# Performance work log

Hardware: AMD Instinct MI355X
Metric: run time of the kernel (lower is better)

Reference implementation:

```python
import jax, jax.numpy as jnp
import numpy as np
import math

D_MODEL = 512
NUM_HEADS = 8
D_K = D_MODEL // NUM_HEADS
MAX_LEN = 500
BATCH = 32
SEQ = 480


def setup_inputs() -> dict:
    key = jax.random.key(0)
    ks = jax.random.split(key, 10)
    s = 0.02
    x = jax.random.normal(ks[0], (BATCH, SEQ, D_MODEL), dtype=jnp.float32)
    wq = jax.random.normal(ks[1], (D_MODEL, D_MODEL), dtype=jnp.float32) * s
    bq = jnp.zeros((D_MODEL,), jnp.float32)
    wk = jax.random.normal(ks[2], (D_MODEL, D_MODEL), dtype=jnp.float32) * s
    bk = jnp.zeros((D_MODEL,), jnp.float32)
    wv = jax.random.normal(ks[3], (D_MODEL, D_MODEL), dtype=jnp.float32) * s
    bv = jnp.zeros((D_MODEL,), jnp.float32)
    wo = jax.random.normal(ks[4], (D_MODEL, D_MODEL), dtype=jnp.float32) * s
    bo = jnp.zeros((D_MODEL,), jnp.float32)
    rel_bias = jax.random.normal(ks[5], (NUM_HEADS, MAX_LEN, MAX_LEN), dtype=jnp.float32) * 0.02
    return {"x": x, "wq": wq, "bq": bq, "wk": wk, "bk": bk, "wv": wv,
            "bv": bv, "wo": wo, "bo": bo, "rel_bias": rel_bias}


def reference(x, wq, bq, wk, bk, wv, bv, wo, bo, rel_bias):
    B, S, D = x.shape
    H, dk = NUM_HEADS, D_K
    scale = math.sqrt(dk)
    # QKV projections -> [B, H, S, dk]
    q = (x @ wq + bq).reshape(B, S, H, dk).transpose(0, 2, 1, 3)
    k = (x @ wk + bk).reshape(B, S, H, dk).transpose(0, 2, 1, 3)
    v = (x @ wv + bv).reshape(B, S, H, dk).transpose(0, 2, 1, 3)
    scores = jnp.einsum('bhqd,bhkd->bhqk', q, k) / scale
    scores = scores + rel_bias[None, :, :S, :S]
    causal = jnp.triu(jnp.ones((S, S), dtype=bool), k=1)  # True where j > i
    scores = jnp.where(causal[None, None], -jnp.inf, scores)
    attn = jax.nn.softmax(scores, axis=-1)
    ctx = jnp.einsum('bhqk,bhkd->bhqd', attn, v)
    ctx = ctx.transpose(0, 2, 1, 3).reshape(B, S, D)
    out = ctx @ wo + bo
    return out, attn.mean(axis=1)
```

## Files before the change

kernel.cpp:

```cpp
#include <hip/hip_runtime.h>
#include <hip/hip_bf16.h>


typedef unsigned short ushort_t;
typedef __attribute__((ext_vector_type(8))) short short8;
typedef __attribute__((ext_vector_type(4))) float floatx4;
typedef __attribute__((ext_vector_type(2))) __fp16 half2v;

#define NB 32
#define NS 480
#define ND 512
#define NH 8
#define NDK 64
#define MAXLEN 500
#define PSTR 36
#define SCL 0.18033688f

__device__ __forceinline__ ushort_t f2bf(float f) {
  union { float f; unsigned u; } v; v.f = f;
  unsigned r = v.u + 0x7FFFu + ((v.u >> 16) & 1u);
  return (ushort_t)(r >> 16);
}

#define GLOAD_LDS16(g, l)                                                      \
  __builtin_amdgcn_global_load_lds(                                            \
      (const __attribute__((address_space(1))) void*)(g),                      \
      (__attribute__((address_space(3))) void*)(l), 16, 0, 0)

__global__ void cvt_x(const float* __restrict__ x, ushort_t* __restrict__ xb) {
  int idx = blockIdx.x * 256 + threadIdx.x;
  float4 v = ((const float4*)x)[idx];
  ushort4 o;
  o.x = f2bf(v.x); o.y = f2bf(v.y); o.z = f2bf(v.z); o.w = f2bf(v.w);
  ((ushort4*)xb)[idx] = o;
}

__global__ void cvt_w(const float* __restrict__ wq, const float* __restrict__ wk,
                      const float* __restrict__ wv, const float* __restrict__ wo,
                      ushort_t* __restrict__ wqT, ushort_t* __restrict__ wkT,
                      ushort_t* __restrict__ wvT, ushort_t* __restrict__ woT) {
  __shared__ float t[32][33];
  int z = blockIdx.z;
  const float* w = (z == 0) ? wq : (z == 1) ? wk : (z == 2) ? wv : wo;
  ushort_t* wT = (z == 0) ? wqT : (z == 1) ? wkT : (z == 2) ? wvT : woT;
  int k0 = blockIdx.x * 32, n0 = blockIdx.y * 32;
  int tx = threadIdx.x & 31, ty = threadIdx.x >> 5;
#pragma unroll
  for (int yy = 0; yy < 4; ++yy)
    t[ty + yy * 8][tx] = w[(k0 + ty + yy * 8) * ND + n0 + tx];
  __syncthreads();
#pragma unroll
  for (int yy = 0; yy < 4; ++yy)
    wT[(n0 + ty + yy * 8) * ND + k0 + tx] = f2bf(t[tx][ty + yy * 8]);
}

__global__ void cvt_rbt(const float* __restrict__ rel_bias, float* __restrict__ rbt) {
  int kt = blockIdx.x, ib = blockIdx.y, h = blockIdx.z;
  int lm = threadIdx.x & 15, ii = threadIdx.x >> 4;
  int i = ib * 16 + ii;
  float f0 = rel_bias[((size_t)h * MAXLEN + i) * MAXLEN + kt * 32 + lm] * 1.44269504f;
  float f1 = rel_bias[((size_t)h * MAXLEN + i) * MAXLEN + kt * 32 + 16 + lm] * 1.44269504f;
  float2 o = {f0, f1};
  *(float2*)&rbt[(((size_t)h * 15 + kt) * NS + i) * 32 + 2 * lm] = o;
}

__global__ __launch_bounds__(256)
void qk_gemm(const ushort_t* __restrict__ xb,
             const ushort_t* __restrict__ wqT, const ushort_t* __restrict__ wkT,
             const float* __restrict__ bq, const float* __restrict__ bk,
             ushort_t* __restrict__ qb, ushort_t* __restrict__ kb) {
  __shared__ __align__(16) ushort_t sA[128 * 64];
  __shared__ __align__(16) ushort_t sB[128 * 64];
  const int tid = threadIdx.x;
  const int wid = tid >> 6, lane = tid & 63;
  const int lm = lane & 15, quad = lane >> 4;
  const int wr = wid >> 1, wc = wid & 1;
  const int row0 = blockIdx.x * 128;
  const int col0 = blockIdx.y * 128;
  const int z = blockIdx.z;
  const ushort_t* Bt = (z == 0) ? wqT : wkT;
  const float* bias = (z == 0) ? bq : bk;

  floatx4 zero4 = {0.f, 0.f, 0.f, 0.f};
  floatx4 acc[4][4];
#pragma unroll
  for (int i = 0; i < 4; ++i)
#pragma unroll
    for (int j = 0; j < 4; ++j) acc[i][j] = zero4;

  for (int k0 = 0; k0 < ND; k0 += 64) {
#pragma unroll
    for (int c = 0; c < 4; ++c) {
      int li = c * 256 + tid;
      int row = li >> 3, kc = li & 7;
      int kcs = kc ^ (row & 7);
      GLOAD_LDS16(xb + (row0 + row) * ND + k0 + kcs * 8, sA + (c * 256 + wid * 64) * 8);
      GLOAD_LDS16(Bt + (col0 + row) * ND + k0 + kcs * 8, sB + (c * 256 + wid * 64) * 8);
    }
    __syncthreads();
#pragma unroll
    for (int h2 = 0; h2 < 2; ++h2) {
      short8 a[4], b[4];
#pragma unroll
      for (int i = 0; i < 4; ++i) {
        int row = wr * 64 + i * 16 + lm;
        a[i] = *(const short8*)&sA[row * 64 + (((h2 << 2) | quad) ^ (lm & 7)) * 8];
      }
#pragma unroll
      for (int j = 0; j < 4; ++j) {
        int row = wc * 64 + j * 16 + lm;
        b[j] = *(const short8*)&sB[row * 64 + (((h2 << 2) | quad) ^ (lm & 7)) * 8];
      }
#pragma unroll
      for (int i = 0; i < 4; ++i)
#pragma unroll
        for (int j = 0; j < 4; ++j)
          acc[i][j] = __builtin_amdgcn_mfma_f32_16x16x32_bf16(a[i], b[j], acc[i][j], 0, 0, 0);
    }
    __syncthreads();
  }

  float bsv[4];
#pragma unroll
  for (int j = 0; j < 4; ++j) bsv[j] = bias[col0 + wc * 64 + j * 16 + lm];

#pragma unroll
  for (int i = 0; i < 4; ++i)
#pragma unroll
    for (int j = 0; j < 4; ++j)
#pragma unroll
      for (int r = 0; r < 4; ++r) {
        int m = row0 + wr * 64 + i * 16 + quad * 4 + r;
        int n = col0 + wc * 64 + j * 16 + lm;
        float val = acc[i][j][r] + bsv[j];
        int bb = m / NS, s = m - bb * NS;
        int h = n >> 6, d = n & 63;
        ushort_t o = f2bf(val);
        if (z == 0) qb[((bb * NH + h) * NS + s) * NDK + d] = o;
        else        kb[((bb * NH + h) * NS + s) * NDK + d] = o;
      }
}

__global__ __launch_bounds__(256)
void v_gemm(const ushort_t* __restrict__ xb, const ushort_t* __restrict__ wvT,
            const float* __restrict__ bv, ushort_t* __restrict__ vtil) {
  __shared__ __align__(16) ushort_t sA[128 * 64];
  __shared__ __align__(16) ushort_t sB[128 * 64];
  const int tid = threadIdx.x;
  const int wid = tid >> 6, lane = tid & 63;
  const int lm = lane & 15, quad = lane >> 4;
  const int wr = wid >> 1, wc = wid & 1;
  const int row0 = blockIdx.x * 128;
  const int col0 = blockIdx.y * 128;
  const int b = blockIdx.z;
  const ushort_t* xbb = xb + (size_t)b * NS * ND;

  floatx4 zero4 = {0.f, 0.f, 0.f, 0.f};
  floatx4 acc[4][4];
#pragma unroll
  for (int i = 0; i < 4; ++i)
#pragma unroll
    for (int j = 0; j < 4; ++j) acc[i][j] = zero4;

  for (int k0 = 0; k0 < ND; k0 += 64) {
#pragma unroll
    for (int c = 0; c < 4; ++c) {
      int li = c * 256 + tid;
      int row = li >> 3, kc = li & 7;
      int kcs = kc ^ (row & 7);
      GLOAD_LDS16(wvT + (row0 + row) * ND + k0 + kcs * 8, sA + (c * 256 + wid * 64) * 8);
      int srow = min(col0 + row, NS - 1);
      GLOAD_LDS16(xbb + srow * ND + k0 + kcs * 8, sB + (c * 256 + wid * 64) * 8);
    }
    __syncthreads();
#pragma unroll
    for (int h2 = 0; h2 < 2; ++h2) {
      short8 a[4], b2[4];
#pragma unroll
      for (int i = 0; i < 4; ++i) {
        int row = wr * 64 + i * 16 + lm;
        a[i] = *(const short8*)&sA[row * 64 + (((h2 << 2) | quad) ^ (lm & 7)) * 8];
      }
#pragma unroll
      for (int j = 0; j < 4; ++j) {
        int row = wc * 64 + j * 16 + lm;
        b2[j] = *(const short8*)&sB[row * 64 + (((h2 << 2) | quad) ^ (lm & 7)) * 8];
      }
#pragma unroll
      for (int i = 0; i < 4; ++i)
#pragma unroll
        for (int j = 0; j < 4; ++j)
          acc[i][j] = __builtin_amdgcn_mfma_f32_16x16x32_bf16(a[i], b2[j], acc[i][j], 0, 0, 0);
    }
    __syncthreads();
  }

#pragma unroll
  for (int i = 0; i < 4; ++i)
#pragma unroll
    for (int r = 0; r < 4; ++r) {
      int m = row0 + wr * 64 + i * 16 + quad * 4 + r;
      float bias = bv[m];
#pragma unroll
      for (int j = 0; j < 4; ++j) {
        int n = col0 + wc * 64 + j * 16 + lm;
        if (n < NS) {
          size_t idx = (((size_t)b * NH + (m >> 6)) * 15 + (n >> 5)) * 2048 +
                       (m & 63) * 32 + (n & 31);
          vtil[idx] = f2bf(acc[i][j][r] + bias);
        }
      }
    }
}

__global__ __launch_bounds__(256, 3)
void flash_attn(const ushort_t* __restrict__ qb, const ushort_t* __restrict__ kb,
                const ushort_t* __restrict__ vtil, const float* __restrict__ rbt,
                ushort_t* __restrict__ ctxb, float* __restrict__ cst,
                uint4* __restrict__ pscr) {
  const int bh = blockIdx.x;
  const int b = bh >> 3, h = bh & 7;
  const int tid = threadIdx.x;
  const int wid = tid >> 6, lane = tid & 63;
  const int lm = lane & 15, quad = lane >> 4;

  __shared__ __align__(16) ushort_t sP[4][32 * PSTR];

  const int t = 14 - (blockIdx.y * 4 + wid);
  if (t < 0) return;
  const int nkt = t + 1;

  const ushort_t* qh = qb + (size_t)bh * NS * NDK;
  const ushort_t* kh = kb + (size_t)bh * NS * NDK;
  const ushort_t* vb = vtil + (size_t)bh * 15 * 2048;
  const float* rb = rbt + (size_t)h * 15 * NS * 32;
  uint4* pp = pscr + ((size_t)(bh * 120 + (t * (t + 1)) / 2)) * 128 + lane;

  short8 aq[2][2];
#pragma unroll
  for (int g = 0; g < 2; ++g) {
    aq[g][0] = *(const short8*)&qh[(t * 32 + g * 16 + lm) * NDK + quad * 8];
    aq[g][1] = *(const short8*)&qh[(t * 32 + g * 16 + lm) * NDK + 32 + quad * 8];
  }

  float lsum[2][4];
  floatx4 O[2][4];
  floatx4 zero4 = {0.f, 0.f, 0.f, 0.f};
#pragma unroll
  for (int g = 0; g < 2; ++g) {
#pragma unroll
    for (int r = 0; r < 4; ++r) lsum[g][r] = 0.f;
#pragma unroll
    for (int jd = 0; jd < 4; ++jd) O[g][jd] = zero4;
  }

  auto loadKV = [&](int kt_, short8& kA0_, short8& kA1_, short8& kB0_,
                    short8& kB1_, short8* vv_) {
    int ra = (kt_ * 32 + lm) * NDK;
    int rbx = ra + 16 * NDK;
    kA0_ = *(const short8*)&kh[ra + quad * 8];
    kA1_ = *(const short8*)&kh[ra + 32 + quad * 8];
    kB0_ = *(const short8*)&kh[rbx + quad * 8];
    kB1_ = *(const short8*)&kh[rbx + 32 + quad * 8];
#pragma unroll
    for (int jd = 0; jd < 4; ++jd)
      vv_[jd] = *(const short8*)&vb[kt_ * 2048 + (jd * 16 + lm) * 32 + quad * 8];
  };

  auto compute = [&](int kt_, short8 kA0_, short8 kA1_, short8 kB0_,
                     short8 kB1_, const short8* vv_) {
    float2 bb[2][4];
#pragma unroll
    for (int g = 0; g < 2; ++g)
#pragma unroll
      for (int r = 0; r < 4; ++r) {
        int i = t * 32 + g * 16 + quad * 4 + r;
        bb[g][r] = *(const float2*)&rb[((size_t)kt_ * NS + i) * 32 + 2 * lm];
      }

    floatx4 sA[2], sB[2];
#pragma unroll
    for (int g = 0; g < 2; ++g) {
      floatx4 s = zero4;
      s = __builtin_amdgcn_mfma_f32_16x16x32_bf16(aq[g][0], kA0_, s, 0, 0, 0);
      s = __builtin_amdgcn_mfma_f32_16x16x32_bf16(aq[g][1], kA1_, s, 0, 0, 0);
      sA[g] = s;
      s = zero4;
      s = __builtin_amdgcn_mfma_f32_16x16x32_bf16(aq[g][0], kB0_, s, 0, 0, 0);
      s = __builtin_amdgcn_mfma_f32_16x16x32_bf16(aq[g][1], kB1_, s, 0, 0, 0);
      sB[g] = s;
    }

    const bool diag = (kt_ == t);
#pragma unroll
    for (int g = 0; g < 2; ++g) {
      unsigned pw[4];
#pragma unroll
      for (int r = 0; r < 4; ++r) {
        float p0 = __builtin_amdgcn_exp2f(fmaf(sA[g][r], SCL, bb[g][r].x));
        float p1 = __builtin_amdgcn_exp2f(fmaf(sB[g][r], SCL, bb[g][r].y));
        if (diag) {
          int i = t * 32 + g * 16 + quad * 4 + r;
          if (kt_ * 32 + lm > i) p0 = 0.f;
          if (kt_ * 32 + 16 + lm > i) p1 = 0.f;
        }
        lsum[g][r] += p0 + p1;
        unsigned pk;
        asm("v_cvt_pk_bf16_f32 %0, %1, %2" : "=v"(pk) : "v"(p0), "v"(p1));
        sP[wid][(g * 16 + quad * 4 + r) * PSTR + lm] = (ushort_t)(pk & 0xffffu);
        sP[wid][(g * 16 + quad * 4 + r) * PSTR + 16 + lm] = (ushort_t)(pk >> 16);
        half2v hp = __builtin_amdgcn_cvt_pkrtz(p0, p1);
        pw[r] = *(unsigned*)&hp;
      }
      uint4 pq = {pw[0], pw[1], pw[2], pw[3]};
      pp[(size_t)kt_ * 128 + g * 64] = pq;
    }

#pragma unroll
    for (int g = 0; g < 2; ++g) {
      short8 ap = *(const short8*)&sP[wid][(g * 16 + lm) * PSTR + quad * 8];
#pragma unroll
      for (int jd = 0; jd < 4; ++jd)
        O[g][jd] = __builtin_amdgcn_mfma_f32_16x16x32_bf16(ap, vv_[jd], O[g][jd], 0, 0, 0);
    }
  };

  short8 kA0a, kA1a, kB0a, kB1a, va[4];
  short8 kA0b, kA1b, kB0b, kB1b, vbf[4];
  loadKV(0, kA0a, kA1a, kB0a, kB1a, va);
  int kt = 0;
  while (true) {
    if (kt + 1 < nkt) loadKV(kt + 1, kA0b, kA1b, kB0b, kB1b, vbf);
    compute(kt, kA0a, kA1a, kB0a, kB1a, va);
    if (++kt >= nkt) break;
    if (kt + 1 < nkt) loadKV(kt + 1, kA0a, kA1a, kB0a, kB1a, va);
    compute(kt, kA0b, kA1b, kB0b, kB1b, vbf);
    if (++kt >= nkt) break;
  }

#pragma unroll
  for (int off = 1; off < 16; off <<= 1)
#pragma unroll
    for (int g = 0; g < 2; ++g)
#pragma unroll
      for (int r = 0; r < 4; ++r) lsum[g][r] += __shfl_xor(lsum[g][r], off, 64);

#pragma unroll
  for (int g = 0; g < 2; ++g) {
    float rinv[4];
#pragma unroll
    for (int r = 0; r < 4; ++r) rinv[r] = 1.f / lsum[g][r];
#pragma unroll
    for (int jd = 0; jd < 4; ++jd)
#pragma unroll
      for (int r = 0; r < 4; ++r) {
        int i = t * 32 + g * 16 + quad * 4 + r;
        ctxb[((size_t)b * NS + i) * ND + h * NDK + jd * 16 + lm] =
            f2bf(O[g][jd][r] * rinv[r]);
      }
    if (lm == 0) {
#pragma unroll
      for (int r = 0; r < 4; ++r) {
        int i = t * 32 + g * 16 + quad * 4 + r;
        cst[(size_t)bh * NS + i] = rinv[r];
      }
    }
  }
}

__global__ __launch_bounds__(64)
void attn_mean_p(const uint4* __restrict__ pscr, const float* __restrict__ cst,
                 float* __restrict__ am) {
  const int b = blockIdx.x, t = blockIdx.y, kt = blockIdx.z;
  const int lane = threadIdx.x;
  const int lm = lane & 15, quad = lane >> 4;
  float* outp = am + ((size_t)b * NS + t * 32) * NS + (size_t)kt * 32;
  if (kt > t) {
#pragma unroll
    for (int g = 0; g < 2; ++g)
#pragma unroll
      for (int r = 0; r < 4; ++r) {
        int row = g * 16 + quad * 4 + r;
        outp[(size_t)row * NS + lm] = 0.f;
        outp[(size_t)row * NS + 16 + lm] = 0.f;
      }
    return;
  }
  const int m = (t * (t + 1)) / 2 + kt;
  float a0[2][4], a1[2][4];
#pragma unroll
  for (int g = 0; g < 2; ++g)
#pragma unroll
    for (int r = 0; r < 4; ++r) { a0[g][r] = 0.f; a1[g][r] = 0.f; }

#pragma unroll
  for (int h = 0; h < NH; ++h) {
    const uint4* pp = pscr + ((size_t)(b * NH + h) * 120 + m) * 128 + lane;
    uint4 q0 = pp[0];
    uint4 q1 = pp[64];
    unsigned pu[8] = {q0.x, q0.y, q0.z, q0.w, q1.x, q1.y, q1.z, q1.w};
    const float* cp = cst + (size_t)(b * NH + h) * NS + t * 32 + quad * 4;
    float4 rv0 = *(const float4*)cp;
    float4 rv1 = *(const float4*)(cp + 16);
    float rv[8] = {rv0.x, rv0.y, rv0.z, rv0.w, rv1.x, rv1.y, rv1.z, rv1.w};
#pragma unroll
    for (int g = 0; g < 2; ++g)
#pragma unroll
      for (int r = 0; r < 4; ++r) {
        half2v hp = *(half2v*)&pu[g * 4 + r];
        a0[g][r] = fmaf((float)hp.x, rv[g * 4 + r], a0[g][r]);
        a1[g][r] = fmaf((float)hp.y, rv[g * 4 + r], a1[g][r]);
      }
  }

#pragma unroll
  for (int g = 0; g < 2; ++g)
#pragma unroll
    for (int r = 0; r < 4; ++r) {
      int row = g * 16 + quad * 4 + r;
      outp[(size_t)row * NS + lm] = a0[g][r] * 0.125f;
      outp[(size_t)row * NS + 16 + lm] = a1[g][r] * 0.125f;
    }
}

__global__ __launch_bounds__(256)
void out_gemm(const ushort_t* __restrict__ ctxb, const ushort_t* __restrict__ woT,
              const float* __restrict__ bo, float* __restrict__ out) {
  __shared__ __align__(16) ushort_t sA[128 * 64];
  __shared__ __align__(16) ushort_t sB[128 * 64];
  const int tid = threadIdx.x;
  const int wid = tid >> 6, lane = tid & 63;
  const int lm = lane & 15, quad = lane >> 4;
  const int wr = wid >> 1, wc = wid & 1;
  const int row0 = blockIdx.x * 128;
  const int col0 = blockIdx.y * 128;

  floatx4 zero4 = {0.f, 0.f, 0.f, 0.f};
  floatx4 acc[4][4];
#pragma unroll
  for (int i = 0; i < 4; ++i)
#pragma unroll
    for (int j = 0; j < 4; ++j) acc[i][j] = zero4;

  for (int k0 = 0; k0 < ND; k0 += 64) {
#pragma unroll
    for (int c = 0; c < 4; ++c) {
      int li = c * 256 + tid;
      int row = li >> 3, kc = li & 7;
      int kcs = kc ^ (row & 7);
      GLOAD_LDS16(ctxb + (row0 + row) * ND + k0 + kcs * 8, sA + (c * 256 + wid * 64) * 8);
      GLOAD_LDS16(woT + (col0 + row) * ND + k0 + kcs * 8, sB + (c * 256 + wid * 64) * 8);
    }
    __syncthreads();
#pragma unroll
    for (int h2 = 0; h2 < 2; ++h2) {
      short8 a[4], b[4];
#pragma unroll
      for (int i = 0; i < 4; ++i) {
        int row = wr * 64 + i * 16 + lm;
        a[i] = *(const short8*)&sA[row * 64 + (((h2 << 2) | quad) ^ (lm & 7)) * 8];
      }
#pragma unroll
      for (int j = 0; j < 4; ++j) {
        int row = wc * 64 + j * 16 + lm;
        b[j] = *(const short8*)&sB[row * 64 + (((h2 << 2) | quad) ^ (lm & 7)) * 8];
      }
#pragma unroll
      for (int i = 0; i < 4; ++i)
#pragma unroll
        for (int j = 0; j < 4; ++j)
          acc[i][j] = __builtin_amdgcn_mfma_f32_16x16x32_bf16(a[i], b[j], acc[i][j], 0, 0, 0);
    }
    __syncthreads();
  }

  float bsv[4];
#pragma unroll
  for (int j = 0; j < 4; ++j) bsv[j] = bo[col0 + wc * 64 + j * 16 + lm];

#pragma unroll
  for (int i = 0; i < 4; ++i)
#pragma unroll
    for (int j = 0; j < 4; ++j)
#pragma unroll
      for (int r = 0; r < 4; ++r) {
        int m = row0 + wr * 64 + i * 16 + quad * 4 + r;
        int n = col0 + wc * 64 + j * 16 + lm;
        out[m * ND + n] = acc[i][j][r] + bsv[j];
      }
}

extern "C" void kernel_launch(void* const* d_in, const int* in_sizes, int n_in,
                              void* d_out, int out_size, void* d_ws, size_t ws_size,
                              hipStream_t stream) {
  const float* x  = (const float*)d_in[0];
  const float* wq = (const float*)d_in[1];
  const float* bq = (const float*)d_in[2];
  const float* wk = (const float*)d_in[3];
  const float* bk = (const float*)d_in[4];
  const float* wv = (const float*)d_in[5];
  const float* bv = (const float*)d_in[6];
  const float* wo = (const float*)d_in[7];
  const float* bo = (const float*)d_in[8];
  const float* rel_bias = (const float*)d_in[9];

  char* w = (char*)d_ws;
  ushort_t* xb  = (ushort_t*)w;
  ushort_t* wqT = (ushort_t*)(w + 15728640);
  ushort_t* wkT = wqT + 262144;
  ushort_t* wvT = wkT + 262144;
  ushort_t* woT = wvT + 262144;
  ushort_t* qb  = (ushort_t*)(w + 15728640 + 4 * 524288);
  ushort_t* kb  = qb + 7864320;
  ushort_t* vtil = kb + 7864320;
  ushort_t* ctxb = vtil + 7864320;
  float* cstat = (float*)(w + 80740352);
  uint4* pscr = (uint4*)(w + 81264640);
  float* rbt = (float*)w;

  float* out0 = (float*)d_out;
  float* attn_mean = out0 + 7864320;

  cvt_x<<<dim3(7680), dim3(256), 0, stream>>>(x, xb);
  cvt_w<<<dim3(16, 16, 4), dim3(256), 0, stream>>>(wq, wk, wv, wo, wqT, wkT, wvT, woT);
  qk_gemm<<<dim3(120, 4, 2), dim3(256), 0, stream>>>(xb, wqT, wkT, bq, bk, qb, kb);
  v_gemm<<<dim3(4, 4, 32), dim3(256), 0, stream>>>(xb, wvT, bv, vtil);
  cvt_rbt<<<dim3(15, 30, 8), dim3(256), 0, stream>>>(rel_bias, rbt);
  flash_attn<<<dim3(256, 4), dim3(256), 0, stream>>>(qb, kb, vtil, rbt, ctxb, cstat, pscr);
  attn_mean_p<<<dim3(32, 15, 15), dim3(64), 0, stream>>>(pscr, cstat, attn_mean);
  out_gemm<<<dim3(120, 4), dim3(256), 0, stream>>>(ctxb, woT, bo, out0);
}
```

Measured before the change: 266.1 us.

## Recompute attention probabilities for head-mean instead of storing fp16 P scratch

flash_attn no longer writes every probability tile to a global fp16 scratch buffer. Instead it stores the per-row log2 of the softmax sum. A new attn_mean_r kernel recomputes QK^T scores with MFMA for all 8 heads, applies the bias and log-sum normalisation, and averages them into the attn-mean output. This trades a large scratch write and read for redundant score computation in the second kernel, and it also saves conversion work in the flash loop.

```diff
diff --git a/kernel.cpp b/kernel.cpp
--- a/kernel.cpp
+++ b/kernel.cpp
@@ -5,7 +5,6 @@
 typedef unsigned short ushort_t;
 typedef __attribute__((ext_vector_type(8))) short short8;
 typedef __attribute__((ext_vector_type(4))) float floatx4;
-typedef __attribute__((ext_vector_type(2))) __fp16 half2v;
 
 #define NB 32
 #define NS 480
@@ -216,8 +215,7 @@
 __global__ __launch_bounds__(256, 3)
 void flash_attn(const ushort_t* __restrict__ qb, const ushort_t* __restrict__ kb,
                 const ushort_t* __restrict__ vtil, const float* __restrict__ rbt,
-                ushort_t* __restrict__ ctxb, float* __restrict__ cst,
-                uint4* __restrict__ pscr) {
+                ushort_t* __restrict__ ctxb, float* __restrict__ cst) {
   const int bh = blockIdx.x;
   const int b = bh >> 3, h = bh & 7;
   const int tid = threadIdx.x;
@@ -234,7 +232,6 @@
   const ushort_t* kh = kb + (size_t)bh * NS * NDK;
   const ushort_t* vb = vtil + (size_t)bh * 15 * 2048;
   const float* rb = rbt + (size_t)h * 15 * NS * 32;
-  uint4* pp = pscr + ((size_t)(bh * 120 + (t * (t + 1)) / 2)) * 128 + lane;
 
   short8 aq[2][2];
 #pragma unroll
@@ -294,7 +291,6 @@
     const bool diag = (kt_ == t);
 #pragma unroll
     for (int g = 0; g < 2; ++g) {
-      unsigned pw[4];
 #pragma unroll
       for (int r = 0; r < 4; ++r) {
         float p0 = __builtin_amdgcn_exp2f(fmaf(sA[g][r], SCL, bb[g][r].x));
@@ -309,11 +305,7 @@
         asm("v_cvt_pk_bf16_f32 %0, %1, %2" : "=v"(pk) : "v"(p0), "v"(p1));
         sP[wid][(g * 16 + quad * 4 + r) * PSTR + lm] = (ushort_t)(pk & 0xffffu);
         sP[wid][(g * 16 + quad * 4 + r) * PSTR + 16 + lm] = (ushort_t)(pk >> 16);
-        half2v hp = __builtin_amdgcn_cvt_pkrtz(p0, p1);
-        pw[r] = *(unsigned*)&hp;
-      }
-      uint4 pq = {pw[0], pw[1], pw[2], pw[3]};
-      pp[(size_t)kt_ * 128 + g * 64] = pq;
+      }
     }
 
 #pragma unroll
@@ -362,65 +354,104 @@
 #pragma unroll
       for (int r = 0; r < 4; ++r) {
         int i = t * 32 + g * 16 + quad * 4 + r;
-        cst[(size_t)bh * NS + i] = rinv[r];
-      }
-    }
-  }
-}
-
-__global__ __launch_bounds__(64)
-void attn_mean_p(const uint4* __restrict__ pscr, const float* __restrict__ cst,
+        cst[((size_t)b * NS + i) * NH + h] = __log2f(lsum[g][r]);
+      }
+    }
+  }
+}
+
+__global__ __launch_bounds__(256)
+void attn_mean_r(const ushort_t* __restrict__ qb, const ushort_t* __restrict__ kb,
+                 const float* __restrict__ rbt, const float* __restrict__ cst,
                  float* __restrict__ am) {
-  const int b = blockIdx.x, t = blockIdx.y, kt = blockIdx.z;
-  const int lane = threadIdx.x;
+  const int b = blockIdx.x;
+  const int tile = blockIdx.y;
+  const int it = tile >> 3, jt = tile & 7;
+  const int tid = threadIdx.x;
+
+  if (jt > it) {
+    int r = tid >> 2;
+    int i = it * 64 + r;
+    if (i < NS) {
+      float4 z = {0.f, 0.f, 0.f, 0.f};
+#pragma unroll
+      for (int cc = 0; cc < 4; ++cc) {
+        int j = jt * 64 + (tid & 3) * 16 + cc * 4;
+        if (j < NS) *(float4*)&am[((size_t)b * NS + i) * NS + j] = z;
+      }
+    }
+    return;
+  }
+
+  const int wid = tid >> 6, lane = tid & 63;
   const int lm = lane & 15, quad = lane >> 4;
-  float* outp = am + ((size_t)b * NS + t * 32) * NS + (size_t)kt * 32;
-  if (kt > t) {
-#pragma unroll
-    for (int g = 0; g < 2; ++g)
-#pragma unroll
-      for (int r = 0; r < 4; ++r) {
-        int row = g * 16 + quad * 4 + r;
-        outp[(size_t)row * NS + lm] = 0.f;
-        outp[(size_t)row * NS + 16 + lm] = 0.f;
-      }
-    return;
-  }
-  const int m = (t * (t + 1)) / 2 + kt;
-  float a0[2][4], a1[2][4];
-#pragma unroll
-  for (int g = 0; g < 2; ++g)
-#pragma unroll
-    for (int r = 0; r < 4; ++r) { a0[g][r] = 0.f; a1[g][r] = 0.f; }
-
-#pragma unroll
+  const int i0 = it * 64 + wid * 16;
+  const int j0 = jt * 64;
+  const bool active = (i0 < NS);
+  const int iq = min(i0 + lm, NS - 1);
+
+  int irow[4], ic[4];
+#pragma unroll
+  for (int r = 0; r < 4; ++r) {
+    irow[r] = i0 + quad * 4 + r;
+    ic[r] = min(irow[r], NS - 1);
+  }
+  int kr[4];
+#pragma unroll
+  for (int jj = 0; jj < 4; ++jj) kr[jj] = min(j0 + jj * 16 + lm, NS - 1);
+  const int kt2g0 = j0 >> 5;
+  const int kt2g1 = min((j0 >> 5) + 1, 14);
+
+  floatx4 zero4 = {0.f, 0.f, 0.f, 0.f};
+  floatx4 acc[4];
+#pragma unroll
+  for (int jj = 0; jj < 4; ++jj) acc[jj] = zero4;
+
   for (int h = 0; h < NH; ++h) {
-    const uint4* pp = pscr + ((size_t)(b * NH + h) * 120 + m) * 128 + lane;
-    uint4 q0 = pp[0];
-    uint4 q1 = pp[64];
-    unsigned pu[8] = {q0.x, q0.y, q0.z, q0.w, q1.x, q1.y, q1.z, q1.w};
-    const float* cp = cst + (size_t)(b * NH + h) * NS + t * 32 + quad * 4;
-    float4 rv0 = *(const float4*)cp;
-    float4 rv1 = *(const float4*)(cp + 16);
-    float rv[8] = {rv0.x, rv0.y, rv0.z, rv0.w, rv1.x, rv1.y, rv1.z, rv1.w};
-#pragma unroll
-    for (int g = 0; g < 2; ++g)
-#pragma unroll
-      for (int r = 0; r < 4; ++r) {
-        half2v hp = *(half2v*)&pu[g * 4 + r];
-        a0[g][r] = fmaf((float)hp.x, rv[g * 4 + r], a0[g][r]);
-        a1[g][r] = fmaf((float)hp.y, rv[g * 4 + r], a1[g][r]);
-      }
-  }
-
-#pragma unroll
-  for (int g = 0; g < 2; ++g)
+    const ushort_t* qh = qb + (size_t)(b * NH + h) * NS * NDK;
+    const ushort_t* kh = kb + (size_t)(b * NH + h) * NS * NDK;
+    short8 qa0 = *(const short8*)&qh[iq * NDK + quad * 8];
+    short8 qa1 = *(const short8*)&qh[iq * NDK + 32 + quad * 8];
+
+    float2 bd[2][4];
 #pragma unroll
     for (int r = 0; r < 4; ++r) {
-      int row = g * 16 + quad * 4 + r;
-      outp[(size_t)row * NS + lm] = a0[g][r] * 0.125f;
-      outp[(size_t)row * NS + 16 + lm] = a1[g][r] * 0.125f;
-    }
+      float c = cst[((size_t)b * NS + ic[r]) * NH + h];
+      float2 b0 = *(const float2*)&rbt[(((size_t)h * 15 + kt2g0) * NS + ic[r]) * 32 + 2 * lm];
+      float2 b1 = *(const float2*)&rbt[(((size_t)h * 15 + kt2g1) * NS + ic[r]) * 32 + 2 * lm];
+      bd[0][r].x = b0.x - c; bd[0][r].y = b0.y - c;
+      bd[1][r].x = b1.x - c; bd[1][r].y = b1.y - c;
+    }
+
+#pragma unroll
+    for (int jj = 0; jj < 4; ++jj) {
+      short8 bk0 = *(const short8*)&kh[kr[jj] * NDK + quad * 8];
+      short8 bk1 = *(const short8*)&kh[kr[jj] * NDK + 32 + quad * 8];
+      floatx4 s = zero4;
+      s = __builtin_amdgcn_mfma_f32_16x16x32_bf16(qa0, bk0, s, 0, 0, 0);
+      s = __builtin_amdgcn_mfma_f32_16x16x32_bf16(qa1, bk1, s, 0, 0, 0);
+      int j = j0 + jj * 16 + lm;
+#pragma unroll
+      for (int r = 0; r < 4; ++r) {
+        float bfv = (jj & 1) ? bd[jj >> 1][r].y : bd[jj >> 1][r].x;
+        float p = __builtin_amdgcn_exp2f(fmaf(s[r], SCL, bfv));
+        if (j > irow[r]) p = 0.f;
+        acc[jj][r] += p;
+      }
+    }
+  }
+
+  if (active) {
+#pragma unroll
+    for (int jj = 0; jj < 4; ++jj) {
+      int j = j0 + jj * 16 + lm;
+      if (j < NS) {
+#pragma unroll
+        for (int r = 0; r < 4; ++r)
+          am[((size_t)b * NS + irow[r]) * NS + j] = acc[jj][r] * 0.125f;
+      }
+    }
+  }
 }
 
 __global__ __launch_bounds__(256)
@@ -515,7 +546,6 @@
   ushort_t* vtil = kb + 7864320;
   ushort_t* ctxb = vtil + 7864320;
   float* cstat = (float*)(w + 80740352);
-  uint4* pscr = (uint4*)(w + 81264640);
   float* rbt = (float*)w;
 
   float* out0 = (float*)d_out;
@@ -526,7 +556,7 @@
   qk_gemm<<<dim3(120, 4, 2), dim3(256), 0, stream>>>(xb, wqT, wkT, bq, bk, qb, kb);
   v_gemm<<<dim3(4, 4, 32), dim3(256), 0, stream>>>(xb, wvT, bv, vtil);
   cvt_rbt<<<dim3(15, 30, 8), dim3(256), 0, stream>>>(rel_bias, rbt);
-  flash_attn<<<dim3(256, 4), dim3(256), 0, stream>>>(qb, kb, vtil, rbt, ctxb, cstat, pscr);
-  attn_mean_p<<<dim3(32, 15, 15), dim3(64), 0, stream>>>(pscr, cstat, attn_mean);
+  flash_attn<<<dim3(256, 4), dim3(256), 0, stream>>>(qb, kb, vtil, rbt, ctxb, cstat);
+  attn_mean_r<<<dim3(32, 64), dim3(256), 0, stream>>>(qb, kb, rbt, cstat, attn_mean);
   out_gemm<<<dim3(120, 4), dim3(256), 0, stream>>>(ctxb, woT, bo, out0);
 }
```

After: 306.9 us. 1.15x slower.

## Drop K/V register double-buffering in flash_attn and add MFMA priority hints

Applied to the files above, without the earlier changes.

Replaces the manual two-slot register prefetch of K and V tiles with a simple per-tile loop that loads and consumes in the same iteration. It wraps the MFMA sections in s_setprio raises so matrix work gets scheduling priority, and removes the minimum-occupancy hint from launch_bounds. The aim is fewer live registers and better interleaving across waves in place of explicit prefetch. The risk is exposed global-load latency per tile, which now relies on other waves to hide it, and possibly lower occupancy without the occupancy bound.

```diff
diff --git a/kernel.cpp b/kernel.cpp
--- a/kernel.cpp
+++ b/kernel.cpp
@@ -213,7 +213,7 @@
     }
 }
 
-__global__ __launch_bounds__(256, 3)
+__global__ __launch_bounds__(256)
 void flash_attn(const ushort_t* __restrict__ qb, const ushort_t* __restrict__ kb,
                 const ushort_t* __restrict__ vtil, const float* __restrict__ rbt,
                 ushort_t* __restrict__ ctxb, float* __restrict__ cst,
@@ -254,44 +254,42 @@
     for (int jd = 0; jd < 4; ++jd) O[g][jd] = zero4;
   }
 
-  auto loadKV = [&](int kt_, short8& kA0_, short8& kA1_, short8& kB0_,
-                    short8& kB1_, short8* vv_) {
-    int ra = (kt_ * 32 + lm) * NDK;
-    int rbx = ra + 16 * NDK;
-    kA0_ = *(const short8*)&kh[ra + quad * 8];
-    kA1_ = *(const short8*)&kh[ra + 32 + quad * 8];
-    kB0_ = *(const short8*)&kh[rbx + quad * 8];
-    kB1_ = *(const short8*)&kh[rbx + 32 + quad * 8];
+  for (int kt = 0; kt < nkt; ++kt) {
+    const int kvA = kt * 32 + lm;
+    const int kvB = kvA + 16;
+    short8 bkA0 = *(const short8*)&kh[kvA * NDK + quad * 8];
+    short8 bkA1 = *(const short8*)&kh[kvA * NDK + 32 + quad * 8];
+    short8 bkB0 = *(const short8*)&kh[kvB * NDK + quad * 8];
+    short8 bkB1 = *(const short8*)&kh[kvB * NDK + 32 + quad * 8];
+    short8 bv2[4];
 #pragma unroll
     for (int jd = 0; jd < 4; ++jd)
-      vv_[jd] = *(const short8*)&vb[kt_ * 2048 + (jd * 16 + lm) * 32 + quad * 8];
-  };
-
-  auto compute = [&](int kt_, short8 kA0_, short8 kA1_, short8 kB0_,
-                     short8 kB1_, const short8* vv_) {
+      bv2[jd] = *(const short8*)&vb[kt * 2048 + (jd * 16 + lm) * 32 + quad * 8];
     float2 bb[2][4];
 #pragma unroll
     for (int g = 0; g < 2; ++g)
 #pragma unroll
       for (int r = 0; r < 4; ++r) {
         int i = t * 32 + g * 16 + quad * 4 + r;
-        bb[g][r] = *(const float2*)&rb[((size_t)kt_ * NS + i) * 32 + 2 * lm];
+        bb[g][r] = *(const float2*)&rb[((size_t)kt * NS + i) * 32 + 2 * lm];
       }
 
     floatx4 sA[2], sB[2];
+    __builtin_amdgcn_s_setprio(1);
 #pragma unroll
     for (int g = 0; g < 2; ++g) {
       floatx4 s = zero4;
-      s = __builtin_amdgcn_mfma_f32_16x16x32_bf16(aq[g][0], kA0_, s, 0, 0, 0);
-      s = __builtin_amdgcn_mfma_f32_16x16x32_bf16(aq[g][1], kA1_, s, 0, 0, 0);
+      s = __builtin_amdgcn_mfma_f32_16x16x32_bf16(aq[g][0], bkA0, s, 0, 0, 0);
+      s = __builtin_amdgcn_mfma_f32_16x16x32_bf16(aq[g][1], bkA1, s, 0, 0, 0);
       sA[g] = s;
       s = zero4;
-      s = __builtin_amdgcn_mfma_f32_16x16x32_bf16(aq[g][0], kB0_, s, 0, 0, 0);
-      s = __builtin_amdgcn_mfma_f32_16x16x32_bf16(aq[g][1], kB1_, s, 0, 0, 0);
+      s = __builtin_amdgcn_mfma_f32_16x16x32_bf16(aq[g][0], bkB0, s, 0, 0, 0);
+      s = __builtin_amdgcn_mfma_f32_16x16x32_bf16(aq[g][1], bkB1, s, 0, 0, 0);
       sB[g] = s;
     }
-
-    const bool diag = (kt_ == t);
+    __builtin_amdgcn_s_setprio(0);
+
+    const bool diag = (kt == t);
 #pragma unroll
     for (int g = 0; g < 2; ++g) {
       unsigned pw[4];
@@ -301,8 +299,8 @@
         float p1 = __builtin_amdgcn_exp2f(fmaf(sB[g][r], SCL, bb[g][r].y));
         if (diag) {
           int i = t * 32 + g * 16 + quad * 4 + r;
-          if (kt_ * 32 + lm > i) p0 = 0.f;
-          if (kt_ * 32 + 16 + lm > i) p1 = 0.f;
+          if (kvA > i) p0 = 0.f;
+          if (kvB > i) p1 = 0.f;
         }
         lsum[g][r] += p0 + p1;
         unsigned pk;
@@ -313,29 +311,18 @@
         pw[r] = *(unsigned*)&hp;
       }
       uint4 pq = {pw[0], pw[1], pw[2], pw[3]};
-      pp[(size_t)kt_ * 128 + g * 64] = pq;
-    }
-
+      pp[(size_t)kt * 128 + g * 64] = pq;
+    }
+
+    __builtin_amdgcn_s_setprio(1);
 #pragma unroll
     for (int g = 0; g < 2; ++g) {
       short8 ap = *(const short8*)&sP[wid][(g * 16 + lm) * PSTR + quad * 8];
 #pragma unroll
       for (int jd = 0; jd < 4; ++jd)
-        O[g][jd] = __builtin_amdgcn_mfma_f32_16x16x32_bf16(ap, vv_[jd], O[g][jd], 0, 0, 0);
-    }
-  };
-
-  short8 kA0a, kA1a, kB0a, kB1a, va[4];
-  short8 kA0b, kA1b, kB0b, kB1b, vbf[4];
-  loadKV(0, kA0a, kA1a, kB0a, kB1a, va);
-  int kt = 0;
-  while (true) {
-    if (kt + 1 < nkt) loadKV(kt + 1, kA0b, kA1b, kB0b, kB1b, vbf);
-    compute(kt, kA0a, kA1a, kB0a, kB1a, va);
-    if (++kt >= nkt) break;
-    if (kt + 1 < nkt) loadKV(kt + 1, kA0a, kA1a, kB0a, kB1a, va);
-    compute(kt, kA0b, kA1b, kB0b, kB1b, vbf);
-    if (++kt >= nkt) break;
+        O[g][jd] = __builtin_amdgcn_mfma_f32_16x16x32_bf16(ap, bv2[jd], O[g][jd], 0, 0, 0);
+    }
+    __builtin_amdgcn_s_setprio(0);
   }
 
 #pragma unroll
```

Result: faster. 230.9 us (-13.2%).
